# Kernel tuning notes

Hardware: AMD Instinct MI355X
Metric: run time of the kernel (lower is better)

Reference implementation:

```python
import jax, jax.numpy as jnp
import numpy as np


def setup_inputs() -> dict:
    key = jax.random.key(0)
    k1, k2 = jax.random.split(key, 2)
    B, C, H, W = 64, 1024, 32, 32
    feature_maps = jax.random.normal(k1, (B, C, H, W), dtype=jnp.float32)
    # 1x1 conv (C -> 1) is just a channel contraction: weight [C], bias [1]
    conv_w = jax.random.normal(k2, (C,), dtype=jnp.float32) * 0.02
    conv_b = jnp.zeros((1,), dtype=jnp.float32)
    M = 768  # int(H * W * drop_rate) = int(1024 * 0.75)
    return {"feature_maps": feature_maps, "conv_w": conv_w, "conv_b": conv_b, "M": M}


def reference(feature_maps, conv_w, conv_b, M):
    # Training-mode ADL forward.
    B, C, H, W = feature_maps.shape
    # 1x1 conv to a single channel + sigmoid -> attention map [B, H, W]
    attn = jax.nn.sigmoid(jnp.einsum('bchw,c->bhw', feature_maps, conv_w) + conv_b[0])
    attn_flat = attn.reshape(B, H * W)
    # drop the top-M most attended spatial locations
    _, topk_idx = jax.lax.top_k(attn_flat, M)            # [B, M]
    drop_mask = jnp.ones_like(attn_flat)
    drop_mask = drop_mask.at[jnp.arange(B)[:, None], topk_idx].set(0.0)
    drop_mask = drop_mask.reshape(B, 1, H, W)
    dropped = feature_maps * drop_mask                   # broadcast over channels
    return dropped, attn.reshape(B, 1, H, W)
```

## Files before the change

kernel.cpp:

```cpp
#include <hip/hip_runtime.h>

#define NB 64
#define NC 1024
#define HW 1024
#define HW4 256
#define CCH 8
#define CPC (NC / CCH)

__global__ void adl_partial_gemv(const float* __restrict__ fm,
                                 const float* __restrict__ w,
                                 float* __restrict__ partial) {
    const int cchunk = blockIdx.x;
    const int b      = blockIdx.y;
    const int t      = threadIdx.x;
    const float4* fm4 = (const float4*)fm;
    float4 acc = make_float4(0.f, 0.f, 0.f, 0.f);
    const int cbase = cchunk * CPC;
    #pragma unroll 4
    for (int ci = 0; ci < CPC; ++ci) {
        const int c = cbase + ci;
        const float4 v = fm4[((size_t)(b * NC + c)) * HW4 + t];
        const float wv = w[c];
        acc.x += v.x * wv;
        acc.y += v.y * wv;
        acc.z += v.z * wv;
        acc.w += v.w * wv;
    }
    ((float4*)partial)[((size_t)(cchunk * NB + b)) * HW4 + t] = acc;
}

__global__ void adl_topk_mask(const float* __restrict__ partial,
                              const float* __restrict__ conv_b,
                              const int* __restrict__ Mptr,
                              float* __restrict__ attn_out,
                              float* __restrict__ mask) {
    __shared__ float a_sh[HW];
    const int b = blockIdx.x;
    const int t = threadIdx.x;
    float s = conv_b[0];
    #pragma unroll
    for (int k = 0; k < CCH; ++k)
        s += partial[((size_t)(k * NB + b)) * HW + t];
    const float a = 1.0f / (1.0f + expf(-s));
    a_sh[t] = a;
    attn_out[(size_t)b * HW + t] = a;
    __syncthreads();
    const int M = *Mptr;
    int r = 0;
    #pragma unroll 8
    for (int j = 0; j < HW; ++j) {
        const float aj = a_sh[j];
        r += (aj > a) || (aj == a && j < t);
    }
    mask[(size_t)b * HW + t] = (r < M) ? 0.0f : 1.0f;
}

__global__ void adl_apply(const float* __restrict__ fm,
                          const float* __restrict__ mask,
                          float* __restrict__ out) {
    const float4* fm4   = (const float4*)fm;
    const float4* mask4 = (const float4*)mask;
    float4* out4        = (float4*)out;
    const size_t total4 = (size_t)NB * NC * HW4;
    const size_t stride = (size_t)gridDim.x * blockDim.x;
    for (size_t i = (size_t)blockIdx.x * blockDim.x + threadIdx.x;
         i < total4; i += stride) {
        const int hw4 = (int)(i & (HW4 - 1));
        const int bc  = (int)(i >> 8);
        const int b   = bc >> 10;
        const float4 m = mask4[b * HW4 + hw4];
        const float4 v = fm4[i];
        float4 o;
        o.x = v.x * m.x;
        o.y = v.y * m.y;
        o.z = v.z * m.z;
        o.w = v.w * m.w;
        out4[i] = o;
    }
}

extern "C" void kernel_launch(void* const* d_in, const int* in_sizes, int n_in,
                              void* d_out, int out_size, void* d_ws, size_t ws_size,
                              hipStream_t stream) {
    const float* fm   = (const float*)d_in[0];
    const float* w    = (const float*)d_in[1];
    const float* bias = (const float*)d_in[2];
    const int*   Mptr = (const int*)d_in[3];

    float* out      = (float*)d_out;
    float* attn_out = out + (size_t)NB * NC * HW;

    float* partial = (float*)d_ws;
    float* mask    = partial + (size_t)CCH * NB * HW;

    adl_partial_gemv<<<dim3(CCH, NB), 256, 0, stream>>>(fm, w, partial);
    adl_topk_mask<<<NB, HW, 0, stream>>>(partial, bias, Mptr, attn_out, mask);
    adl_apply<<<2048, 256, 0, stream>>>(fm, mask, out);
}
```

Measured before the change: 196.9 us.

## Split channel reduction wider, parallelize top-k ranking, use nontemporal output stores

When workspace allows, the channel GEMV is split into 16 chunks instead of 8, doubling block count to raise occupancy during the reduction read of the feature map. The rank/top-k kernel now runs 4 blocks of 256 threads per batch, each recomputing the summed logits into shared memory and ranking a quarter of positions. Ranking compares pre-sigmoid logits with vectorized shared reads. The apply kernel uses nontemporal stores for the large output. The trade-offs are redundant partial-sum reads in the top-k kernel, and that ties between distinct logits that round to the same sigmoid value may now be ordered differently.

New measurement: 179.0 us. 9.1% less time.

```diff
diff --git a/kernel.cpp b/kernel.cpp
--- a/kernel.cpp
+++ b/kernel.cpp
@@ -1,81 +1,84 @@
 #include <hip/hip_runtime.h>
+
+typedef float f32x4 __attribute__((ext_vector_type(4)));
 
 #define NB 64
 #define NC 1024
 #define HW 1024
 #define HW4 256
-#define CCH 8
-#define CPC (NC / CCH)
 
+template<int CPC>
 __global__ void adl_partial_gemv(const float* __restrict__ fm,
                                  const float* __restrict__ w,
                                  float* __restrict__ partial) {
     const int cchunk = blockIdx.x;
     const int b      = blockIdx.y;
     const int t      = threadIdx.x;
-    const float4* fm4 = (const float4*)fm;
-    float4 acc = make_float4(0.f, 0.f, 0.f, 0.f);
+    const f32x4* fm4 = (const f32x4*)fm;
+    f32x4 acc = {0.f, 0.f, 0.f, 0.f};
     const int cbase = cchunk * CPC;
-    #pragma unroll 4
+    #pragma unroll 8
     for (int ci = 0; ci < CPC; ++ci) {
         const int c = cbase + ci;
-        const float4 v = fm4[((size_t)(b * NC + c)) * HW4 + t];
-        const float wv = w[c];
-        acc.x += v.x * wv;
-        acc.y += v.y * wv;
-        acc.z += v.z * wv;
-        acc.w += v.w * wv;
+        const f32x4 v = fm4[((size_t)(b * NC + c)) * HW4 + t];
+        acc += v * w[c];
     }
-    ((float4*)partial)[((size_t)(cchunk * NB + b)) * HW4 + t] = acc;
+    ((f32x4*)partial)[((size_t)(cchunk * NB + b)) * HW4 + t] = acc;
 }
 
 __global__ void adl_topk_mask(const float* __restrict__ partial,
                               const float* __restrict__ conv_b,
                               const int* __restrict__ Mptr,
+                              int ncch,
                               float* __restrict__ attn_out,
                               float* __restrict__ mask) {
-    __shared__ float a_sh[HW];
-    const int b = blockIdx.x;
-    const int t = threadIdx.x;
-    float s = conv_b[0];
+    __shared__ f32x4 s_sh4[HW4];
+    float* s_sh = (float*)s_sh4;
+    const int slice = blockIdx.x;
+    const int b     = blockIdx.y;
+    const int tid   = threadIdx.x;
+    const float bias = conv_b[0];
     #pragma unroll
-    for (int k = 0; k < CCH; ++k)
-        s += partial[((size_t)(k * NB + b)) * HW + t];
-    const float a = 1.0f / (1.0f + expf(-s));
-    a_sh[t] = a;
-    attn_out[(size_t)b * HW + t] = a;
+    for (int q = 0; q < 4; ++q) {
+        const int t = q * 256 + tid;
+        float s = bias;
+        for (int k = 0; k < ncch; ++k)
+            s += partial[((size_t)(k * NB + b)) * HW + t];
+        s_sh[t] = s;
+    }
     __syncthreads();
+    const int t = slice * 256 + tid;
+    const float sv = s_sh[t];
     const int M = *Mptr;
     int r = 0;
-    #pragma unroll 8
-    for (int j = 0; j < HW; ++j) {
-        const float aj = a_sh[j];
-        r += (aj > a) || (aj == a && j < t);
+    #pragma unroll 4
+    for (int j4 = 0; j4 < HW4; ++j4) {
+        const f32x4 v = s_sh4[j4];
+        const int j = j4 * 4;
+        r += (v.x > sv) || (v.x == sv && (j + 0) < t);
+        r += (v.y > sv) || (v.y == sv && (j + 1) < t);
+        r += (v.z > sv) || (v.z == sv && (j + 2) < t);
+        r += (v.w > sv) || (v.w == sv && (j + 3) < t);
     }
+    attn_out[(size_t)b * HW + t] = 1.0f / (1.0f + expf(-sv));
     mask[(size_t)b * HW + t] = (r < M) ? 0.0f : 1.0f;
 }
 
 __global__ void adl_apply(const float* __restrict__ fm,
                           const float* __restrict__ mask,
                           float* __restrict__ out) {
-    const float4* fm4   = (const float4*)fm;
-    const float4* mask4 = (const float4*)mask;
-    float4* out4        = (float4*)out;
+    const f32x4* fm4   = (const f32x4*)fm;
+    const f32x4* mask4 = (const f32x4*)mask;
+    f32x4* out4        = (f32x4*)out;
     const size_t total4 = (size_t)NB * NC * HW4;
     const size_t stride = (size_t)gridDim.x * blockDim.x;
     for (size_t i = (size_t)blockIdx.x * blockDim.x + threadIdx.x;
          i < total4; i += stride) {
         const int hw4 = (int)(i & (HW4 - 1));
-        const int bc  = (int)(i >> 8);
-        const int b   = bc >> 10;
-        const float4 m = mask4[b * HW4 + hw4];
-        const float4 v = fm4[i];
-        float4 o;
-        o.x = v.x * m.x;
-        o.y = v.y * m.y;
-        o.z = v.z * m.z;
-        o.w = v.w * m.w;
-        out4[i] = o;
+        const int b   = (int)(i >> 18);
+        const f32x4 m = mask4[b * HW4 + hw4];
+        const f32x4 v = fm4[i];
+        __builtin_nontemporal_store(v * m, &out4[i]);
     }
 }
 
@@ -90,10 +93,15 @@
     float* out      = (float*)d_out;
     float* attn_out = out + (size_t)NB * NC * HW;
 
+    const size_t need16 = ((size_t)16 * NB * HW + (size_t)NB * HW) * sizeof(float);
+    const int ncch = (ws_size >= need16) ? 16 : 8;
     float* partial = (float*)d_ws;
-    float* mask    = partial + (size_t)CCH * NB * HW;
+    float* mask    = partial + (size_t)ncch * NB * HW;
 
-    adl_partial_gemv<<<dim3(CCH, NB), 256, 0, stream>>>(fm, w, partial);
-    adl_topk_mask<<<NB, HW, 0, stream>>>(partial, bias, Mptr, attn_out, mask);
+    if (ncch == 16)
+        adl_partial_gemv<NC / 16><<<dim3(16, NB), 256, 0, stream>>>(fm, w, partial);
+    else
+        adl_partial_gemv<NC / 8><<<dim3(8, NB), 256, 0, stream>>>(fm, w, partial);
+    adl_topk_mask<<<dim3(4, NB), 256, 0, stream>>>(partial, bias, Mptr, ncch, attn_out, mask);
     adl_apply<<<2048, 256, 0, stream>>>(fm, mask, out);
 }
```
